# Performance work log

Hardware: AMD Instinct MI355X
Metric: run time of the kernel (lower is better)

Reference implementation:

```python
import jax, jax.numpy as jnp
import numpy as np

B, T = 2, 2048
V, D, H, HS, L = 32000, 512, 8, 64, 4
FF = 4 * D
EPS = 1e-5


def layer_norm(x, g, b):
    mu = jnp.mean(x, axis=-1, keepdims=True)
    var = jnp.mean((x - mu) ** 2, axis=-1, keepdims=True)
    return (x - mu) * jax.lax.rsqrt(var + EPS) * g + b


def setup_inputs() -> dict:
    key = jax.random.key(0)
    ks = iter(jax.random.split(key, 32))
    s = 0.02
    n = lambda shape: jax.random.normal(next(ks), shape, dtype=jnp.float32) * s
    inp = {
        "idx": jax.random.randint(next(ks), (B, T), 0, V),
        "targets": jax.random.randint(next(ks), (B, T), 0, V),
        "tok_emb": n((V, D)),
        "pos_emb": n((T, D)),
        "ln1_g": jnp.ones((L, D)), "ln1_b": jnp.zeros((L, D)),
        "Wq": n((L, H, D, HS)), "Wk": n((L, H, D, HS)), "Wv": n((L, H, D, HS)),
        "Wo": n((L, H * HS, D)), "bo": jnp.zeros((L, D)),
        "ln2_g": jnp.ones((L, D)), "ln2_b": jnp.zeros((L, D)),
        "W1": n((L, D, FF)), "b1": jnp.zeros((L, FF)),
        "W2": n((L, FF, D)), "b2": jnp.zeros((L, D)),
        "lnf_g": jnp.ones((D,)), "lnf_b": jnp.zeros((D,)),
        "Wout": n((D, V)), "bout": jnp.zeros((V,)),
    }
    return inp


def reference(idx, targets, tok_emb, pos_emb, ln1_g, ln1_b, Wq, Wk, Wv, Wo, bo,
              ln2_g, ln2_b, W1, b1, W2, b2, lnf_g, lnf_b, Wout, bout):
    x = tok_emb[idx] + pos_emb[None, :idx.shape[1], :]  # [B,T,D]
    causal = jnp.tril(jnp.ones((T, T), dtype=bool))
    scale = 1.0 / jnp.sqrt(jnp.float32(D))  # NOTE: source divides by sqrt(C)=sqrt(n_embeddings)
    for l in range(L):
        h = layer_norm(x, ln1_g[l], ln1_b[l])
        q = jnp.einsum('btd,hde->bhte', h, Wq[l])
        k = jnp.einsum('btd,hde->bhte', h, Wk[l])
        v = jnp.einsum('btd,hde->bhte', h, Wv[l])
        w = jnp.einsum('bhte,bhse->bhts', q, k) * scale
        w = jnp.where(causal[None, None], w, -jnp.inf)
        w = jax.nn.softmax(w, axis=-1)  # dropout is identity in eval
        attn = jnp.einsum('bhts,bhse->bhte', w, v)
        attn = attn.transpose(0, 2, 1, 3).reshape(x.shape[0], T, H * HS)
        x = x + attn @ Wo[l] + bo[l]
        h2 = layer_norm(x, ln2_g[l], ln2_b[l])
        x = x + jax.nn.relu(h2 @ W1[l] + b1[l]) @ W2[l] + b2[l]
    x = layer_norm(x, lnf_g, lnf_b)
    logits = x @ Wout + bout  # [B,T,V]
    logp = jax.nn.log_softmax(logits, axis=-1)
    tgt_logp = jnp.take_along_axis(logp, targets[..., None], axis=-1)[..., 0]
    loss = -jnp.mean(tgt_logp)
    return loss, logits
```

## Files before the change

### kernel.cpp

```cpp
#include <hip/hip_runtime.h>
#include <hip/hip_bf16.h>
#include <math.h>

#define TT 2048
#define BB 2
#define VV 32000
#define DD 512
#define HH 8
#define HSS 64
#define LL 4
#define FF_ 2048
#define NBLK_V (VV / 128)

using bf16x8 = __attribute__((ext_vector_type(8))) short;
using floatx4 = __attribute__((ext_vector_type(4))) float;

__device__ __forceinline__ ushort f2bf(float f) {
    __hip_bfloat16 b = __float2bfloat16(f);
    return *reinterpret_cast<ushort*>(&b);
}
__device__ __forceinline__ float bf2f(ushort u) {
    union { unsigned int i; float f; } x; x.i = ((unsigned int)u) << 16; return x.f;
}
__device__ __forceinline__ void gload16(const void* g, void* l) {
    __builtin_amdgcn_global_load_lds(
        (const __attribute__((address_space(1))) void*)g,
        (__attribute__((address_space(3))) void*)l, 16, 0, 0);
}

__global__ __launch_bounds__(64)
void embed_kernel(const int* __restrict__ idx, const float* __restrict__ tok,
                  const float* __restrict__ pos, float* __restrict__ x)
{
    int row = blockIdx.x;
    int t = row & (TT - 1);
    int tokid = idx[row];
    int lane = threadIdx.x;
    const float4* tp = (const float4*)(tok + (size_t)tokid * DD);
    const float4* pp = (const float4*)(pos + (size_t)t * DD);
    float4* xp = (float4*)(x + (size_t)row * DD);
    int i0 = lane * 2;
    float4 a = tp[i0],   b4 = pp[i0];
    float4 c = tp[i0+1], d4 = pp[i0+1];
    xp[i0]   = make_float4(a.x + b4.x, a.y + b4.y, a.z + b4.z, a.w + b4.w);
    xp[i0+1] = make_float4(c.x + d4.x, c.y + d4.y, c.z + d4.z, c.w + d4.w);
}

__global__ __launch_bounds__(256)
void ln_kernel(const float* __restrict__ x, const float* __restrict__ g,
               const float* __restrict__ b, ushort* __restrict__ out)
{
    int wave = threadIdx.x >> 6;
    int lane = threadIdx.x & 63;
    int row  = blockIdx.x * 4 + wave;
    const float* xr = x + (size_t)row * DD;
    float4 v0 = *(const float4*)(xr + lane * 8);
    float4 v1 = *(const float4*)(xr + lane * 8 + 4);
    float s = v0.x + v0.y + v0.z + v0.w + v1.x + v1.y + v1.z + v1.w;
    float q = v0.x*v0.x + v0.y*v0.y + v0.z*v0.z + v0.w*v0.w
            + v1.x*v1.x + v1.y*v1.y + v1.z*v1.z + v1.w*v1.w;
    #pragma unroll
    for (int off = 32; off; off >>= 1) {
        s += __shfl_xor(s, off);
        q += __shfl_xor(q, off);
    }
    float mu  = s * (1.0f / DD);
    float var = q * (1.0f / DD) - mu * mu;
    float rs  = rsqrtf(var + 1e-5f);
    float4 g0 = *(const float4*)(g + lane * 8);
    float4 g1 = *(const float4*)(g + lane * 8 + 4);
    float4 b0 = *(const float4*)(b + lane * 8);
    float4 b1 = *(const float4*)(b + lane * 8 + 4);
    union { ushort u[8]; uint4 v; } pk;
    pk.u[0] = f2bf((v0.x - mu) * rs * g0.x + b0.x);
    pk.u[1] = f2bf((v0.y - mu) * rs * g0.y + b0.y);
    pk.u[2] = f2bf((v0.z - mu) * rs * g0.z + b0.z);
    pk.u[3] = f2bf((v0.w - mu) * rs * g0.w + b0.w);
    pk.u[4] = f2bf((v1.x - mu) * rs * g1.x + b1.x);
    pk.u[5] = f2bf((v1.y - mu) * rs * g1.y + b1.y);
    pk.u[6] = f2bf((v1.z - mu) * rs * g1.z + b1.z);
    pk.u[7] = f2bf((v1.w - mu) * rs * g1.w + b1.w);
    *(uint4*)(out + (size_t)row * DD + lane * 8) = pk.v;
}

__global__ __launch_bounds__(256)
void transpose_cvt(const float* __restrict__ in, ushort* __restrict__ out,
                   int N, int K, long inStrideZ, long outStrideZ)
{
    __shared__ float t[64][65];
    in  += (size_t)blockIdx.z * inStrideZ;
    out += (size_t)blockIdx.z * outStrideZ;
    const int n0 = blockIdx.x * 64, k0 = blockIdx.y * 64;
    const int r = threadIdx.x >> 2;
    const int c = (threadIdx.x & 3) * 16;
    #pragma unroll
    for (int j = 0; j < 16; j += 4) {
        float4 v = *(const float4*)&in[(size_t)(k0 + r) * N + n0 + c + j];
        t[r][c + j + 0] = v.x; t[r][c + j + 1] = v.y;
        t[r][c + j + 2] = v.z; t[r][c + j + 3] = v.w;
    }
    __syncthreads();
    union { ushort u[8]; uint4 v; } pk;
    ushort* orow = out + (size_t)(n0 + r) * K + k0 + c;
    #pragma unroll
    for (int half = 0; half < 2; ++half) {
        #pragma unroll
        for (int j = 0; j < 8; ++j) pk.u[j] = f2bf(t[c + half * 8 + j][r]);
        *(uint4*)(orow + half * 8) = pk.v;
    }
}

__global__ __launch_bounds__(256)
void qkv_transpose(const float* __restrict__ Wq, const float* __restrict__ Wk,
                   const float* __restrict__ Wv, ushort* __restrict__ out)
{
    __shared__ float t[64][65];
    const int z = blockIdx.y;
    const int sel = z >> 5, l = (z >> 3) & 3, h = z & 7;
    const float* in = (sel == 0 ? Wq : sel == 1 ? Wk : Wv)
                      + (size_t)l * (HH * DD * HSS) + (size_t)h * (DD * HSS);
    ushort* ob = out + (size_t)l * (3 * DD * DD) + (size_t)sel * (DD * DD)
                     + (size_t)h * (HSS * DD);
    const int d0 = blockIdx.x * 64;
    const int r = threadIdx.x >> 2;
    const int c = (threadIdx.x & 3) * 16;
    #pragma unroll
    for (int j = 0; j < 16; j += 4) {
        float4 v = *(const float4*)&in[(size_t)(d0 + r) * HSS + c + j];
        t[r][c + j + 0] = v.x; t[r][c + j + 1] = v.y;
        t[r][c + j + 2] = v.z; t[r][c + j + 3] = v.w;
    }
    __syncthreads();
    union { ushort u[8]; uint4 v; } pk;
    ushort* orow = ob + (size_t)r * DD + d0 + c;
    #pragma unroll
    for (int half = 0; half < 2; ++half) {
        #pragma unroll
        for (int j = 0; j < 8; ++j) pk.u[j] = f2bf(t[c + half * 8 + j][r]);
        *(uint4*)(orow + half * 8) = pk.v;
    }
}

__global__ __launch_bounds__(512, 2)
void mfma_gemm_logits(const ushort* __restrict__ A, int lda,
                      const ushort* __restrict__ Bt, int ldb,
                      float* __restrict__ Cf, int ldc,
                      const float* __restrict__ bias,
                      int K,
                      float* __restrict__ smax, float* __restrict__ ssum, int nblks)
{
    __shared__ ushort As[32 * 512];
    __shared__ ushort Bs[16 * 512];
    __shared__ float sstat[2][256][2];

    const int bxx = blockIdx.x, byy = blockIdx.y;
    const int m0 = byy << 8, n0 = bxx << 7;
    const int tid = threadIdx.x, w = tid >> 6, lane = tid & 63;
    const int wm = w >> 1, wn = w & 1;
    const int l15 = lane & 15, lk = lane >> 4;

    floatx4 acc[4][4] = {};

    for (int k0 = 0; k0 < K; k0 += 64) {
        #pragma unroll
        for (int i = 0; i < 4; ++i) {
            int c = 4 * w + i;
            int cg = c >> 1, ckh = c & 1;
            gload16(A + (size_t)(m0 + cg * 16 + l15) * lda + k0 + lk * 8 + ckh * 32,
                    &As[c * 512]);
        }
        #pragma unroll
        for (int i = 0; i < 2; ++i) {
            int c = 2 * w + i;
            int cg = c >> 1, ckh = c & 1;
            gload16(Bt + (size_t)(n0 + cg * 16 + l15) * ldb + k0 + lk * 8 + ckh * 32,
                    &Bs[c * 512]);
        }
        __syncthreads();
        #pragma unroll
        for (int kh = 0; kh < 2; ++kh) {
            bf16x8 af[4], bfr[4];
            #pragma unroll
            for (int mi = 0; mi < 4; ++mi)
                af[mi] = *(const bf16x8*)&As[(((wm * 4 + mi) * 2 + kh) * 64 + lane) * 8];
            #pragma unroll
            for (int ni = 0; ni < 4; ++ni)
                bfr[ni] = *(const bf16x8*)&Bs[(((wn * 4 + ni) * 2 + kh) * 64 + lane) * 8];
            #pragma unroll
            for (int mi = 0; mi < 4; ++mi)
                #pragma unroll
                for (int ni = 0; ni < 4; ++ni)
                    acc[mi][ni] = __builtin_amdgcn_mfma_f32_16x16x32_bf16(
                        af[mi], bfr[ni], acc[mi][ni], 0, 0, 0);
        }
        __syncthreads();
    }

    #pragma unroll
    for (int mi = 0; mi < 4; ++mi)
        #pragma unroll
        for (int ni = 0; ni < 4; ++ni) {
            float bv = bias[n0 + wn * 64 + ni * 16 + l15];
            #pragma unroll
            for (int r = 0; r < 4; ++r) acc[mi][ni][r] += bv;
        }

    #pragma unroll
    for (int mi = 0; mi < 4; ++mi) {
        #pragma unroll
        for (int r = 0; r < 4; ++r) {
            int grow = m0 + wm * 64 + mi * 16 + lk * 4 + r;
            #pragma unroll
            for (int ni = 0; ni < 4; ++ni)
                Cf[(size_t)grow * ldc + n0 + wn * 64 + ni * 16 + l15] = acc[mi][ni][r];
        }
    }

    #pragma unroll
    for (int mi = 0; mi < 4; ++mi) {
        #pragma unroll
        for (int r = 0; r < 4; ++r) {
            float m4 = fmaxf(fmaxf(acc[mi][0][r], acc[mi][1][r]),
                             fmaxf(acc[mi][2][r], acc[mi][3][r]));
            m4 = fmaxf(m4, __shfl_xor(m4, 1));
            m4 = fmaxf(m4, __shfl_xor(m4, 2));
            m4 = fmaxf(m4, __shfl_xor(m4, 4));
            m4 = fmaxf(m4, __shfl_xor(m4, 8));
            float s4 = 0.f;
            #pragma unroll
            for (int ni = 0; ni < 4; ++ni) s4 += __expf(acc[mi][ni][r] - m4);
            s4 += __shfl_xor(s4, 1);
            s4 += __shfl_xor(s4, 2);
            s4 += __shfl_xor(s4, 4);
            s4 += __shfl_xor(s4, 8);
            if (l15 == 0) {
                int R = wm * 64 + mi * 16 + lk * 4 + r;
                sstat[0][R][wn] = m4;
                sstat[1][R][wn] = s4;
            }
        }
    }
    __syncthreads();
    if (tid < 256) {
        float ma = sstat[0][tid][0], mb = sstat[0][tid][1];
        float M = fmaxf(ma, mb);
        float S = sstat[1][tid][0] * __expf(ma - M)
                + sstat[1][tid][1] * __expf(mb - M);
        smax[(size_t)(m0 + tid) * nblks + bxx] = M;
        ssum[(size_t)(m0 + tid) * nblks + bxx] = S;
    }
}

__global__ __launch_bounds__(256, 2)
void mfma_gemm_db(const ushort* __restrict__ A, int lda,
                  const ushort* __restrict__ Bt, int ldb,
                  float* __restrict__ Cf, ushort* __restrict__ Cbf, int ldc,
                  const float* __restrict__ bias,
                  const float* __restrict__ resid, int ldres,
                  int K, int relu)
{
    __shared__ ushort st[2][2][8192];

    const int m0 = blockIdx.y << 7, n0 = blockIdx.x << 7;
    const int tid = threadIdx.x, w = tid >> 6, lane = tid & 63;
    const int wm = w >> 1, wn = w & 1;
    const int l15 = lane & 15, lk = lane >> 4;
    const int nt = K >> 6;

    auto STAGE = [&](int t, int p) {
        const int k0 = t << 6;
        #pragma unroll
        for (int i = 0; i < 4; ++i) {
            int c = 4 * w + i;
            int cg = c >> 3, cmi = (c >> 1) & 3, ckh = c & 1;
            gload16(A + (size_t)(m0 + cg * 64 + cmi * 16 + l15) * lda
                      + k0 + lk * 8 + ckh * 32, &st[p][0][c * 512]);
            gload16(Bt + (size_t)(n0 + cg * 64 + cmi * 16 + l15) * ldb
                       + k0 + lk * 8 + ckh * 32, &st[p][1][c * 512]);
        }
    };

    floatx4 acc[4][4] = {};
    STAGE(0, 0);

    for (int t = 0; t < nt; ++t) {
        const int p = t & 1;
        if (t + 1 < nt) {
            STAGE(t + 1, p ^ 1);
            asm volatile("s_waitcnt vmcnt(8)" ::: "memory");
        } else {
            asm volatile("s_waitcnt vmcnt(0)" ::: "memory");
        }
        __builtin_amdgcn_s_barrier();
        __builtin_amdgcn_sched_barrier(0);
        #pragma unroll
        for (int kh = 0; kh < 2; ++kh) {
            bf16x8 af[4], bfr[4];
            #pragma unroll
            for (int mi = 0; mi < 4; ++mi)
                af[mi] = *(const bf16x8*)&st[p][0][((wm * 8 + mi * 2 + kh) * 64 + lane) * 8];
            #pragma unroll
            for (int ni = 0; ni < 4; ++ni)
                bfr[ni] = *(const bf16x8*)&st[p][1][((wn * 8 + ni * 2 + kh) * 64 + lane) * 8];
            #pragma unroll
            for (int mi = 0; mi < 4; ++mi)
                #pragma unroll
                for (int ni = 0; ni < 4; ++ni)
                    acc[mi][ni] = __builtin_amdgcn_mfma_f32_16x16x32_bf16(
                        af[mi], bfr[ni], acc[mi][ni], 0, 0, 0);
        }
        __builtin_amdgcn_sched_barrier(0);
        __builtin_amdgcn_s_barrier();
    }

    #pragma unroll
    for (int mi = 0; mi < 4; ++mi)
        #pragma unroll
        for (int ni = 0; ni < 4; ++ni)
            #pragma unroll
            for (int r = 0; r < 4; ++r) {
                float v = acc[mi][ni][r];
                if (bias) v += bias[n0 + wn * 64 + ni * 16 + l15];
                if (relu) v = fmaxf(v, 0.0f);
                acc[mi][ni][r] = v;
            }

    #pragma unroll
    for (int mi = 0; mi < 4; ++mi) {
        #pragma unroll
        for (int r = 0; r < 4; ++r) {
            int grow = m0 + wm * 64 + mi * 16 + lk * 4 + r;
            #pragma unroll
            for (int ni = 0; ni < 4; ++ni) {
                int gcol = n0 + wn * 64 + ni * 16 + l15;
                float v = acc[mi][ni][r];
                if (resid) v += resid[(size_t)grow * ldres + gcol];
                if (Cbf) Cbf[(size_t)grow * ldc + gcol] = f2bf(v);
                else     Cf [(size_t)grow * ldc + gcol] = v;
            }
        }
    }
}

__global__ __launch_bounds__(256, 3)
void mfma_gemm_db64(const ushort* __restrict__ A, int lda,
                    const ushort* __restrict__ Bt, int ldb,
                    float* __restrict__ Cf, ushort* __restrict__ Cbf, int ldc,
                    const float* __restrict__ bias,
                    const float* __restrict__ resid, int ldres,
                    int K, int relu)
{
    __shared__ ushort stA[2][8 * 512];
    __shared__ ushort stB[2][16 * 512];

    const int m0 = blockIdx.y << 6, n0 = blockIdx.x << 7;
    const int tid = threadIdx.x, w = tid >> 6, lane = tid & 63;
    const int l15 = lane & 15, lk = lane >> 4;
    const int nt = K >> 6;

    auto STAGE = [&](int t, int p) {
        const int k0 = t << 6;
        #pragma unroll
        for (int i = 0; i < 2; ++i) {
            int c = 2 * w + i;
            int cmi = c >> 1, ckh = c & 1;
            gload16(A + (size_t)(m0 + cmi * 16 + l15) * lda
                      + k0 + lk * 8 + ckh * 32, &stA[p][c * 512]);
        }
        #pragma unroll
        for (int i = 0; i < 4; ++i) {
            int c = 4 * w + i;
            int cnj = c >> 1, ckh = c & 1;
            gload16(Bt + (size_t)(n0 + cnj * 16 + l15) * ldb
                       + k0 + lk * 8 + ckh * 32, &stB[p][c * 512]);
        }
    };

    floatx4 acc[4][2] = {};
    STAGE(0, 0);

    for (int t = 0; t < nt; ++t) {
        const int p = t & 1;
        if (t + 1 < nt) {
            STAGE(t + 1, p ^ 1);
            asm volatile("s_waitcnt vmcnt(6)" ::: "memory");
        } else {
            asm volatile("s_waitcnt vmcnt(0)" ::: "memory");
        }
        __builtin_amdgcn_s_barrier();
        __builtin_amdgcn_sched_barrier(0);
        #pragma unroll
        for (int kh = 0; kh < 2; ++kh) {
            bf16x8 af[4], bfr[2];
            #pragma unroll
            for (int mi = 0; mi < 4; ++mi)
                af[mi] = *(const bf16x8*)&stA[p][((mi * 2 + kh) * 64 + lane) * 8];
            #pragma unroll
            for (int ni = 0; ni < 2; ++ni)
                bfr[ni] = *(const bf16x8*)&stB[p][(((w * 2 + ni) * 2 + kh) * 64 + lane) * 8];
            #pragma unroll
            for (int mi = 0; mi < 4; ++mi)
                #pragma unroll
                for (int ni = 0; ni < 2; ++ni)
                    acc[mi][ni] = __builtin_amdgcn_mfma_f32_16x16x32_bf16(
                        af[mi], bfr[ni], acc[mi][ni], 0, 0, 0);
        }
        __builtin_amdgcn_sched_barrier(0);
        __builtin_amdgcn_s_barrier();
    }

    #pragma unroll
    for (int mi = 0; mi < 4; ++mi)
        #pragma unroll
        for (int ni = 0; ni < 2; ++ni)
            #pragma unroll
            for (int r = 0; r < 4; ++r) {
                float v = acc[mi][ni][r];
                if (bias) v += bias[n0 + w * 32 + ni * 16 + l15];
                if (relu) v = fmaxf(v, 0.0f);
                acc[mi][ni][r] = v;
            }

    #pragma unroll
    for (int mi = 0; mi < 4; ++mi) {
        #pragma unroll
        for (int r = 0; r < 4; ++r) {
            int grow = m0 + mi * 16 + lk * 4 + r;
            #pragma unroll
            for (int ni = 0; ni < 2; ++ni) {
                int gcol = n0 + w * 32 + ni * 16 + l15;
                float v = acc[mi][ni][r];
                if (resid) v += resid[(size_t)grow * ldres + gcol];
                if (Cbf) Cbf[(size_t)grow * ldc + gcol] = f2bf(v);
                else     Cf [(size_t)grow * ldc + gcol] = v;
            }
        }
    }
}

__global__ __launch_bounds__(256)
void attn_mfma_kernel(const ushort* __restrict__ qkv, ushort* __restrict__ out)
{
    __shared__ ushort Vt[64][72];
    __shared__ ushort Pl[64][72];

    const int z = blockIdx.y, b = z >> 3, h = z & 7;
    const int q0 = blockIdx.x << 6;
    const int tid = threadIdx.x;
    const int w = tid >> 6, lane = tid & 63;
    const int l15 = lane & 15, g = lane >> 4;
    const float scale = 0.04419417382415922f;

    const int vkey = tid & 63, vd0 = (tid >> 6) * 16;

    bf16x8 qf0, qf1;
    {
        const ushort* qp = qkv + ((size_t)(b * TT + q0 + 16 * w + l15)) * 1536
                               + h * HSS + g * 8;
        qf0 = *(const bf16x8*)qp;
        qf1 = *(const bf16x8*)(qp + 32);
    }

    floatx4 acc_o[4] = {};
    float lreg[4] = {};

    for (int s0 = 0; s0 <= q0; s0 += 64) {
        __syncthreads();
        {
            const ushort* vp = qkv + ((size_t)(b * TT + s0 + vkey)) * 1536
                                   + 1024 + h * HSS + vd0;
            bf16x8 v0 = *(const bf16x8*)vp;
            bf16x8 v1 = *(const bf16x8*)(vp + 8);
            #pragma unroll
            for (int j = 0; j < 8; ++j) {
                Vt[vd0 + j][vkey]     = (ushort)v0[j];
                Vt[vd0 + 8 + j][vkey] = (ushort)v1[j];
            }
        }

        floatx4 s4[4] = {};
        #pragma unroll
        for (int kb = 0; kb < 4; ++kb) {
            const ushort* kp = qkv + ((size_t)(b * TT + s0 + kb * 16 + l15)) * 1536
                                   + 512 + h * HSS + g * 8;
            bf16x8 kf0 = *(const bf16x8*)kp;
            bf16x8 kf1 = *(const bf16x8*)(kp + 32);
            s4[kb] = __builtin_amdgcn_mfma_f32_16x16x32_bf16(qf0, kf0, s4[kb], 0, 0, 0);
            s4[kb] = __builtin_amdgcn_mfma_f32_16x16x32_bf16(qf1, kf1, s4[kb], 0, 0, 0);
        }

        const bool diag = (s0 == q0);
        #pragma unroll
        for (int r = 0; r < 4; ++r) {
            const int qrow = q0 + 16 * w + g * 4 + r;
            #pragma unroll
            for (int kb = 0; kb < 4; ++kb) {
                float xs = s4[kb][r] * scale;
                if (diag && (s0 + kb * 16 + l15) > qrow) xs = -1e30f;
                float p = __expf(xs);
                lreg[r] += p;
                Pl[16 * w + g * 4 + r][kb * 16 + l15] = f2bf(p);
            }
        }
        __syncthreads();

        bf16x8 pa0 = *(const bf16x8*)&Pl[16 * w + l15][g * 8];
        bf16x8 pa1 = *(const bf16x8*)&Pl[16 * w + l15][g * 8 + 32];
        #pragma unroll
        for (int db = 0; db < 4; ++db) {
            bf16x8 vb0 = *(const bf16x8*)&Vt[db * 16 + l15][g * 8];
            bf16x8 vb1 = *(const bf16x8*)&Vt[db * 16 + l15][g * 8 + 32];
            acc_o[db] = __builtin_amdgcn_mfma_f32_16x16x32_bf16(pa0, vb0, acc_o[db], 0, 0, 0);
            acc_o[db] = __builtin_amdgcn_mfma_f32_16x16x32_bf16(pa1, vb1, acc_o[db], 0, 0, 0);
        }
    }

    #pragma unroll
    for (int r = 0; r < 4; ++r) {
        float l = lreg[r];
        l += __shfl_xor(l, 1);
        l += __shfl_xor(l, 2);
        l += __shfl_xor(l, 4);
        l += __shfl_xor(l, 8);
        float inv = 1.0f / l;
        ushort* op = out + ((size_t)(b * TT + q0 + 16 * w + g * 4 + r)) * DD + h * HSS;
        #pragma unroll
        for (int db = 0; db < 4; ++db)
            op[db * 16 + l15] = f2bf(acc_o[db][r] * inv);
    }
}

__global__ __launch_bounds__(256)
void rowloss_finalize(const float* __restrict__ logits, const int* __restrict__ targets,
                      const float* __restrict__ smax, const float* __restrict__ ssum,
                      float* __restrict__ rowloss)
{
    const int wv = threadIdx.x >> 6, lane = threadIdx.x & 63;
    const int row = blockIdx.x * 4 + wv;
    const float* mrow = smax + (size_t)row * NBLK_V;
    const float* srow = ssum + (size_t)row * NBLK_V;
    float M = -1e30f;
    for (int i = lane; i < NBLK_V; i += 64) M = fmaxf(M, mrow[i]);
    #pragma unroll
    for (int off = 32; off; off >>= 1) M = fmaxf(M, __shfl_xor(M, off));
    float S = 0.f;
    for (int i = lane; i < NBLK_V; i += 64) S += srow[i] * __expf(mrow[i] - M);
    #pragma unroll
    for (int off = 32; off; off >>= 1) S += __shfl_xor(S, off);
    if (lane == 0)
        rowloss[row] = -(logits[(size_t)row * VV + targets[row]] - M - logf(S));
}

__global__ __launch_bounds__(256)
void loss_finalize(const float* __restrict__ rowloss, float* __restrict__ out)
{
    __shared__ float red[256];
    float s = 0.f;
    for (int i = threadIdx.x; i < BB * TT; i += 256) s += rowloss[i];
    red[threadIdx.x] = s; __syncthreads();
    for (int s2 = 128; s2; s2 >>= 1) {
        if (threadIdx.x < s2) red[threadIdx.x] += red[threadIdx.x + s2];
        __syncthreads();
    }
    if (threadIdx.x == 0) out[0] = red[0] * (1.0f / (BB * TT));
}

extern "C" void kernel_launch(void* const* d_in, const int* in_sizes, int n_in,
                              void* d_out, int out_size, void* d_ws, size_t ws_size,
                              hipStream_t stream) {
    const int*   idx     = (const int*)  d_in[0];
    const int*   targets = (const int*)  d_in[1];
    const float* tok_emb = (const float*)d_in[2];
    const float* pos_emb = (const float*)d_in[3];
    const float* ln1_g   = (const float*)d_in[4];
    const float* ln1_b   = (const float*)d_in[5];
    const float* Wq      = (const float*)d_in[6];
    const float* Wk      = (const float*)d_in[7];
    const float* Wv      = (const float*)d_in[8];
    const float* Wo      = (const float*)d_in[9];
    const float* bo      = (const float*)d_in[10];
    const float* ln2_g   = (const float*)d_in[11];
    const float* ln2_b   = (const float*)d_in[12];
    const float* W1      = (const float*)d_in[13];
    const float* b1      = (const float*)d_in[14];
    const float* W2      = (const float*)d_in[15];
    const float* b2      = (const float*)d_in[16];
    const float* lnf_g   = (const float*)d_in[17];
    const float* lnf_b   = (const float*)d_in[18];
    const float* Wout    = (const float*)d_in[19];
    const float* bout    = (const float*)d_in[20];

    float* outf   = (float*)d_out;
    float* logits = outf + 1;

    const size_t ROW = (size_t)BB * TT;

    float*  x     = (float*)d_ws;
    ushort* h_bf  = (ushort*)(x + ROW * DD);
    ushort* Woutt = h_bf + ROW * DD;
    float*  rowloss = (float*)(Woutt + (size_t)VV * DD);
    float* smax = x;
    float* ssum = x + ROW * NBLK_V;

    ushort* sc     = (ushort*)(outf + 8);
    ushort* qkv_bf = sc;
    ushort* ff_bf  = qkv_bf + ROW * 1536;
    ushort* Wqkvt  = ff_bf + ROW * FF_;
    ushort* Wot    = Wqkvt + (size_t)LL * 1536 * DD;
    ushort* W1t    = Wot   + (size_t)LL * DD * DD;
    ushort* W2t    = W1t   + (size_t)LL * FF_ * DD;

    qkv_transpose<<<dim3(8, 96), 256, 0, stream>>>(Wq, Wk, Wv, Wqkvt);
    transpose_cvt<<<dim3(8, 8, LL),  256, 0, stream>>>(Wo,   Wot,   DD,  DD,  (long)DD*DD,   (long)DD*DD);
    transpose_cvt<<<dim3(32, 8, LL), 256, 0, stream>>>(W1,   W1t,   FF_, DD,  (long)DD*FF_,  (long)DD*FF_);
    transpose_cvt<<<dim3(8, 32, LL), 256, 0, stream>>>(W2,   W2t,   DD,  FF_, (long)FF_*DD,  (long)FF_*DD);
    transpose_cvt<<<dim3(500, 8, 1), 256, 0, stream>>>(Wout, Woutt, VV,  DD,  0, 0);

    embed_kernel<<<ROW, 64, 0, stream>>>(idx, tok_emb, pos_emb, x);

    for (int l = 0; l < LL; ++l) {
        ln_kernel<<<ROW / 4, 256, 0, stream>>>(x, ln1_g + l * DD, ln1_b + l * DD, h_bf);

        mfma_gemm_db<<<dim3(1536 / 128, ROW / 128), 256, 0, stream>>>(
            h_bf, DD, Wqkvt + (size_t)l * 1536 * DD, DD,
            nullptr, qkv_bf, 1536, nullptr, nullptr, 0, DD, 0);

        attn_mfma_kernel<<<dim3(TT / 64, BB * HH), 256, 0, stream>>>(qkv_bf, h_bf);

        mfma_gemm_db64<<<dim3(DD / 128, ROW / 64), 256, 0, stream>>>(
            h_bf, DD, Wot + (size_t)l * DD * DD, DD,
            x, nullptr, DD, bo + l * DD, x, DD, DD, 0);

        ln_kernel<<<ROW / 4, 256, 0, stream>>>(x, ln2_g + l * DD, ln2_b + l * DD, h_bf);

        mfma_gemm_db<<<dim3(FF_ / 128, ROW / 128), 256, 0, stream>>>(
            h_bf, DD, W1t + (size_t)l * FF_ * DD, DD,
            nullptr, ff_bf, FF_, b1 + l * FF_, nullptr, 0, DD, 1);

        mfma_gemm_db64<<<dim3(DD / 128, ROW / 64), 256, 0, stream>>>(
            ff_bf, FF_, W2t + (size_t)l * DD * FF_, FF_,
            x, nullptr, DD, b2 + l * DD, x, DD, FF_, 0);
    }

    ln_kernel<<<ROW / 4, 256, 0, stream>>>(x, lnf_g, lnf_b, h_bf);

    mfma_gemm_logits<<<dim3(VV / 128, ROW / 256), 512, 0, stream>>>(
        h_bf, DD, Woutt, DD,
        logits, VV, bout, DD,
        smax, ssum, NBLK_V);

    rowloss_finalize<<<ROW / 4, 256, 0, stream>>>(logits, targets, smax, ssum, rowloss);
    loss_finalize<<<1, 256, 0, stream>>>(rowloss, outf);
}
```

Baseline: 1.278 ms.

## Pre-transpose V in global memory and prefetch K tiles in attention

Adds a separate kernel that writes V into a per-head transposed global buffer, so the attention kernel can load V tiles into LDS with direct 16-byte async loads into an XOR-swizzled layout. This replaces the scalar transposing LDS stores it did before. The attention kernel also register double-buffers the K fragments for the next key block while the current block is processed. The cost is an extra kernel launch and V round-trip per layer, plus higher register pressure from holding 16 K fragments.

```diff
diff --git a/kernel.cpp b/kernel.cpp
--- a/kernel.cpp
+++ b/kernel.cpp
@@ -141,6 +141,29 @@
     }
 }
 
+__global__ __launch_bounds__(256)
+void v_transpose(const ushort* __restrict__ qkv, ushort* __restrict__ vt)
+{
+    __shared__ ushort t[64][72];
+    const int z = blockIdx.y;
+    const int t0 = blockIdx.x * 64;
+    const int b = z >> 3, h = z & 7;
+    const int tr = threadIdx.x >> 2;
+    const int dc = (threadIdx.x & 3) * 16;
+    const ushort* src = qkv + ((size_t)(b * TT + t0 + tr)) * 1536 + 1024 + h * HSS + dc;
+    *(uint4*)&t[tr][dc]     = *(const uint4*)src;
+    *(uint4*)&t[tr][dc + 8] = *(const uint4*)(src + 8);
+    __syncthreads();
+    const int dr = threadIdx.x >> 2;
+    const int tc = (threadIdx.x & 3) * 16;
+    ushort* dst = vt + ((size_t)z * 64 + dr) * TT + t0 + tc;
+    union { ushort u[8]; uint4 v; } p0, p1;
+    #pragma unroll
+    for (int j = 0; j < 8; ++j) { p0.u[j] = t[tc + j][dr]; p1.u[j] = t[tc + 8 + j][dr]; }
+    *(uint4*)dst       = p0.v;
+    *(uint4*)(dst + 8) = p1.v;
+}
+
 __global__ __launch_bounds__(512, 2)
 void mfma_gemm_logits(const ushort* __restrict__ A, int lda,
                       const ushort* __restrict__ Bt, int ldb,
@@ -439,9 +462,10 @@
 }
 
 __global__ __launch_bounds__(256)
-void attn_mfma_kernel(const ushort* __restrict__ qkv, ushort* __restrict__ out)
-{
-    __shared__ ushort Vt[64][72];
+void attn_mfma_kernel(const ushort* __restrict__ qkv, const ushort* __restrict__ vt,
+                      ushort* __restrict__ out)
+{
+    __shared__ ushort Vl[64 * 64];
     __shared__ ushort Pl[64][72];
 
     const int z = blockIdx.y, b = z >> 3, h = z & 7;
@@ -450,8 +474,7 @@
     const int w = tid >> 6, lane = tid & 63;
     const int l15 = lane & 15, g = lane >> 4;
     const float scale = 0.04419417382415922f;
-
-    const int vkey = tid & 63, vd0 = (tid >> 6) * 16;
+    const ushort* vbase = vt + (size_t)z * 64 * TT;
 
     bf16x8 qf0, qf1;
     {
@@ -461,32 +484,47 @@
         qf1 = *(const bf16x8*)(qp + 32);
     }
 
+    bf16x8 kc[8], kn[8];
+    {
+        #pragma unroll
+        for (int kb = 0; kb < 4; ++kb) {
+            const ushort* kp = qkv + ((size_t)(b * TT + kb * 16 + l15)) * 1536
+                                   + 512 + h * HSS + g * 8;
+            kc[kb * 2]     = *(const bf16x8*)kp;
+            kc[kb * 2 + 1] = *(const bf16x8*)(kp + 32);
+        }
+    }
+
     floatx4 acc_o[4] = {};
     float lreg[4] = {};
 
     for (int s0 = 0; s0 <= q0; s0 += 64) {
         __syncthreads();
-        {
-            const ushort* vp = qkv + ((size_t)(b * TT + s0 + vkey)) * 1536
-                                   + 1024 + h * HSS + vd0;
-            bf16x8 v0 = *(const bf16x8*)vp;
-            bf16x8 v1 = *(const bf16x8*)(vp + 8);
-            #pragma unroll
-            for (int j = 0; j < 8; ++j) {
-                Vt[vd0 + j][vkey]     = (ushort)v0[j];
-                Vt[vd0 + 8 + j][vkey] = (ushort)v1[j];
+        #pragma unroll
+        for (int i = 0; i < 2; ++i) {
+            const int cbase = (w * 2 + i) * 64;
+            const int c = cbase + lane;
+            const int row = c >> 3;
+            const int kg = (c & 7) ^ (row & 7);
+            gload16(vbase + (size_t)row * TT + s0 + kg * 8, &Vl[cbase * 8]);
+        }
+
+        floatx4 s4[4] = {};
+        #pragma unroll
+        for (int kb = 0; kb < 4; ++kb) {
+            s4[kb] = __builtin_amdgcn_mfma_f32_16x16x32_bf16(qf0, kc[kb*2],   s4[kb], 0, 0, 0);
+            s4[kb] = __builtin_amdgcn_mfma_f32_16x16x32_bf16(qf1, kc[kb*2+1], s4[kb], 0, 0, 0);
+        }
+
+        const bool more = (s0 + 64 <= q0);
+        if (more) {
+            #pragma unroll
+            for (int kb = 0; kb < 4; ++kb) {
+                const ushort* kp = qkv + ((size_t)(b * TT + s0 + 64 + kb * 16 + l15)) * 1536
+                                       + 512 + h * HSS + g * 8;
+                kn[kb * 2]     = *(const bf16x8*)kp;
+                kn[kb * 2 + 1] = *(const bf16x8*)(kp + 32);
             }
-        }
-
-        floatx4 s4[4] = {};
-        #pragma unroll
-        for (int kb = 0; kb < 4; ++kb) {
-            const ushort* kp = qkv + ((size_t)(b * TT + s0 + kb * 16 + l15)) * 1536
-                                   + 512 + h * HSS + g * 8;
-            bf16x8 kf0 = *(const bf16x8*)kp;
-            bf16x8 kf1 = *(const bf16x8*)(kp + 32);
-            s4[kb] = __builtin_amdgcn_mfma_f32_16x16x32_bf16(qf0, kf0, s4[kb], 0, 0, 0);
-            s4[kb] = __builtin_amdgcn_mfma_f32_16x16x32_bf16(qf1, kf1, s4[kb], 0, 0, 0);
         }
 
         const bool diag = (s0 == q0);
@@ -508,10 +546,16 @@
         bf16x8 pa1 = *(const bf16x8*)&Pl[16 * w + l15][g * 8 + 32];
         #pragma unroll
         for (int db = 0; db < 4; ++db) {
-            bf16x8 vb0 = *(const bf16x8*)&Vt[db * 16 + l15][g * 8];
-            bf16x8 vb1 = *(const bf16x8*)&Vt[db * 16 + l15][g * 8 + 32];
+            const int row = db * 16 + l15;
+            const bf16x8 vb0 = *(const bf16x8*)&Vl[row * 64 + ((g       ^ (row & 7)) * 8)];
+            const bf16x8 vb1 = *(const bf16x8*)&Vl[row * 64 + (((g + 4) ^ (row & 7)) * 8)];
             acc_o[db] = __builtin_amdgcn_mfma_f32_16x16x32_bf16(pa0, vb0, acc_o[db], 0, 0, 0);
             acc_o[db] = __builtin_amdgcn_mfma_f32_16x16x32_bf16(pa1, vb1, acc_o[db], 0, 0, 0);
+        }
+
+        if (more) {
+            #pragma unroll
+            for (int i = 0; i < 8; ++i) kc[i] = kn[i];
         }
     }
 
@@ -609,6 +653,7 @@
     ushort* Wot    = Wqkvt + (size_t)LL * 1536 * DD;
     ushort* W1t    = Wot   + (size_t)LL * DD * DD;
     ushort* W2t    = W1t   + (size_t)LL * FF_ * DD;
+    ushort* vt_g   = W2t   + (size_t)LL * DD * FF_;
 
     qkv_transpose<<<dim3(8, 96), 256, 0, stream>>>(Wq, Wk, Wv, Wqkvt);
     transpose_cvt<<<dim3(8, 8, LL),  256, 0, stream>>>(Wo,   Wot,   DD,  DD,  (long)DD*DD,   (long)DD*DD);
@@ -625,7 +670,9 @@
             h_bf, DD, Wqkvt + (size_t)l * 1536 * DD, DD,
             nullptr, qkv_bf, 1536, nullptr, nullptr, 0, DD, 0);
 
-        attn_mfma_kernel<<<dim3(TT / 64, BB * HH), 256, 0, stream>>>(qkv_bf, h_bf);
+        v_transpose<<<dim3(TT / 64, BB * HH), 256, 0, stream>>>(qkv_bf, vt_g);
+
+        attn_mfma_kernel<<<dim3(TT / 64, BB * HH), 256, 0, stream>>>(qkv_bf, vt_g, h_bf);
 
         mfma_gemm_db64<<<dim3(DD / 128, ROW / 64), 256, 0, stream>>>(
             h_bf, DD, Wot + (size_t)l * DD * DD, DD,
```

Result: faster. 1.227 ms (median of 2 runs) (-4.0%).
